# Kernel tuning notes

Hardware: AMD Instinct MI355X
Metric: run time of the kernel (lower is better)

Reference implementation:

```python
import jax, jax.numpy as jnp
import numpy as np

B, NT, S, D, VOCAB = 32, 1024, 4096, 512, 2545


def setup_inputs() -> dict:
    key = jax.random.key(0)
    k1, k2, k3, k4 = jax.random.split(key, 4)
    raw = jax.random.randint(k1, (B, NT), 0, VOCAB, dtype=jnp.int32)
    # per-sample text lengths; trailing positions padded with -1 (-> id 0 after +1)
    text_lens = jax.random.randint(k2, (B,), NT // 2, NT + 1, dtype=jnp.int32)
    pos = jnp.arange(NT, dtype=jnp.int32)[None, :]
    text = jnp.where(pos < text_lens[:, None], raw, -1).astype(jnp.int32)
    # per-sample target (audio) lengths; pin max to S so max_seq_len is static
    seq_len = jax.random.randint(k3, (B,), S // 2, S + 1, dtype=jnp.int32)
    seq_len = seq_len.at[0].set(S)
    # nn.Embedding default init: N(0, 1)
    W_embed = jax.random.normal(k4, (VOCAB + 1, D), dtype=jnp.float32)
    return {"text": text, "seq_len": seq_len, "W_embed": W_embed}


def _upsample_one(emb_i, L, A):
    # emb_i: [S, D]; valid tokens occupy the prefix of length L.
    # Replicates the torch length-regulator: token j repeated base times,
    # plus one extra repeat for the last `remainder` tokens (j >= L - r).
    t = jnp.arange(emb_i.shape[0], dtype=jnp.int32)
    Ls = jnp.maximum(L, 1)
    base = A // Ls
    r = A % Ls
    split = (L - r) * base  # output positions < split map to blocks of size `base`
    j = jnp.where(
        t < split,
        t // jnp.maximum(base, 1),
        (L - r) + (t - split) // (base + 1),
    )
    j = jnp.clip(j, 0, emb_i.shape[0] - 1)
    out = emb_i[j]  # gather from prefix (valid indices are contiguous from 0)
    ok = (t < A)[:, None] & (L > 0) & (A > 0)
    return jnp.where(ok, out, 0.0)


def reference(text, seq_len, W_embed):
    ids = text + 1                                        # [B, NT], pads (-1) -> 0
    ids = jnp.pad(ids, ((0, 0), (0, S - NT)))             # pad to max_seq_len with 0
    pos = jnp.arange(S, dtype=jnp.int32)[None, :]
    valid_pos = pos < seq_len[:, None]                    # [B, S]
    ids = jnp.where(valid_pos, ids, 0)
    text_mask = ids == 0                                  # padding mask
    emb = W_embed[ids]                                    # [B, S, D] embedding lookup
    emb = jnp.where(valid_pos[..., None], emb, 0.0)
    text_lens = jnp.sum(~text_mask, axis=1).astype(jnp.int32)
    return jax.vmap(_upsample_one)(emb, text_lens, seq_len)
```

## Files before the change

### kernel.cpp

```cpp
#include <hip/hip_runtime.h>

#define BB 32
#define NT 1024
#define SS 4096
#define DD 512
#define D4 128

typedef float f32x4 __attribute__((ext_vector_type(4)));

__global__ void prep_kernel(const int* __restrict__ text,
                            const int* __restrict__ seq_len,
                            int4* __restrict__ params) {
    int b = blockIdx.x;
    int tid = threadIdx.x;
    int cnt = 0;
    for (int k = tid; k < NT; k += 256)
        cnt += (text[b * NT + k] >= 0) ? 1 : 0;
    for (int off = 32; off > 0; off >>= 1)
        cnt += __shfl_down(cnt, off);
    __shared__ int s[4];
    if ((tid & 63) == 0) s[tid >> 6] = cnt;
    __syncthreads();
    if (tid == 0) {
        int L = s[0] + s[1] + s[2] + s[3];
        int A = seq_len[b];
        int Ls = (L > 0) ? L : 1;
        int base = A / Ls;
        int rr = A - base * Ls;
        int split = (L - rr) * base;
        params[b] = make_int4(L, base, rr, split);
    }
}

__global__ void __launch_bounds__(256) upsample_kernel(
        const int* __restrict__ text,
        const int* __restrict__ seq_len,
        const f32x4* __restrict__ W4,
        const int4* __restrict__ params,
        f32x4* __restrict__ out4) {
    int idx = blockIdx.x * 256 + threadIdx.x;
    int d4  = idx & (D4 - 1);
    int row = idx >> 7;
    int t   = row & (SS - 1);
    int b   = row >> 12;

    int A = seq_len[b];
    f32x4 v = (f32x4)(0.0f);
    if (t < A) {
        int4 p = params[b];
        int L = p.x, base = p.y, rr = p.z, split = p.w;
        if (L > 0) {
            int j;
            if (t < split) {
                int bb = (base > 0) ? base : 1;
                j = t / bb;
            } else {
                j = (L - rr) + (t - split) / (base + 1);
            }
            if (j > SS - 1) j = SS - 1;
            if (j < 0) j = 0;
            int tok = text[b * NT + j] + 1;
            v = W4[(long)tok * D4 + d4];
        }
    }
    __builtin_nontemporal_store(v, &out4[idx]);
}

extern "C" void kernel_launch(void* const* d_in, const int* in_sizes, int n_in,
                              void* d_out, int out_size, void* d_ws, size_t ws_size,
                              hipStream_t stream) {
    const int* text    = (const int*)d_in[0];
    const int* seq_len = (const int*)d_in[1];
    const f32x4* W4    = (const f32x4*)d_in[2];
    f32x4* out4        = (f32x4*)d_out;
    int4* params       = (int4*)d_ws;

    prep_kernel<<<BB, 256, 0, stream>>>(text, seq_len, params);

    int total = BB * SS * D4;
    upsample_kernel<<<total / 256, 256, 0, stream>>>(text, seq_len, W4, params, out4);
}
```

Before: 52.57 us.

## Fuse length-count prep into upsample kernel via per-wave ballot search

Removes the separate prep kernel and computes each sample's text length inside every wavefront using two ballot passes that locate the first -1 pad. This relies on padding being a contiguous suffix, which the input setup guarantees. Each wave now handles one output row with two vec4 loads and stores per lane, instead of one vec4 per thread. This saves a kernel launch and the dependency between kernels, but adds redundant text reads and ballots per row.

```diff
diff --git a/kernel.cpp b/kernel.cpp
--- a/kernel.cpp
+++ b/kernel.cpp
@@ -1,69 +1,61 @@
 #include <hip/hip_runtime.h>
 
 #define BB 32
-#define NT 1024
+#define NTT 1024
 #define SS 4096
-#define DD 512
 #define D4 128
 
 typedef float f32x4 __attribute__((ext_vector_type(4)));
 
-__global__ void prep_kernel(const int* __restrict__ text,
-                            const int* __restrict__ seq_len,
-                            int4* __restrict__ params) {
-    int b = blockIdx.x;
-    int tid = threadIdx.x;
-    int cnt = 0;
-    for (int k = tid; k < NT; k += 256)
-        cnt += (text[b * NT + k] >= 0) ? 1 : 0;
-    for (int off = 32; off > 0; off >>= 1)
-        cnt += __shfl_down(cnt, off);
-    __shared__ int s[4];
-    if ((tid & 63) == 0) s[tid >> 6] = cnt;
-    __syncthreads();
-    if (tid == 0) {
-        int L = s[0] + s[1] + s[2] + s[3];
-        int A = seq_len[b];
-        int Ls = (L > 0) ? L : 1;
-        int base = A / Ls;
-        int rr = A - base * Ls;
-        int split = (L - rr) * base;
-        params[b] = make_int4(L, base, rr, split);
-    }
-}
-
-__global__ void __launch_bounds__(256) upsample_kernel(
+__global__ void __launch_bounds__(256) fused_upsample_kernel(
         const int* __restrict__ text,
         const int* __restrict__ seq_len,
         const f32x4* __restrict__ W4,
-        const int4* __restrict__ params,
         f32x4* __restrict__ out4) {
-    int idx = blockIdx.x * 256 + threadIdx.x;
-    int d4  = idx & (D4 - 1);
-    int row = idx >> 7;
-    int t   = row & (SS - 1);
-    int b   = row >> 12;
+    int wid  = (blockIdx.x << 2) + (threadIdx.x >> 6);
+    int lane = threadIdx.x & 63;
+    int t = wid & (SS - 1);
+    int b = wid >> 12;
+
+    const int* trow = text + b * NTT;
+
+    int v1 = trow[lane << 4];
+    unsigned long long m1 = __ballot(v1 < 0);
+    int lo;
+    if (m1 == 0ull) {
+        lo = NTT - 16;
+    } else {
+        int p = __builtin_ctzll(m1);
+        lo = (p == 0) ? 0 : ((p - 1) << 4);
+    }
+    int k2 = lo + lane;
+    int v2 = (k2 < NTT) ? trow[k2] : -1;
+    unsigned long long m2 = __ballot(v2 < 0);
+    int L = lo + __builtin_ctzll(m2);
 
     int A = seq_len[b];
-    f32x4 v = (f32x4)(0.0f);
-    if (t < A) {
-        int4 p = params[b];
-        int L = p.x, base = p.y, rr = p.z, split = p.w;
-        if (L > 0) {
-            int j;
-            if (t < split) {
-                int bb = (base > 0) ? base : 1;
-                j = t / bb;
-            } else {
-                j = (L - rr) + (t - split) / (base + 1);
-            }
-            if (j > SS - 1) j = SS - 1;
-            if (j < 0) j = 0;
-            int tok = text[b * NT + j] + 1;
-            v = W4[(long)tok * D4 + d4];
+
+    f32x4 va = (f32x4)(0.0f);
+    f32x4 vb = (f32x4)(0.0f);
+    if (t < A && L > 0) {
+        int base  = (int)((unsigned)A / (unsigned)L);
+        int rr    = A - base * L;
+        int split = (L - rr) * base;
+        int j;
+        if (t < split) {
+            j = (int)((unsigned)t / (unsigned)base);
+        } else {
+            j = (L - rr) + (int)((unsigned)(t - split) / (unsigned)(base + 1));
         }
+        if (j > L - 1) j = L - 1;
+        int tok = trow[j] + 1;
+        const f32x4* wr = W4 + (long)tok * D4;
+        va = wr[lane];
+        vb = wr[lane + 64];
     }
-    __builtin_nontemporal_store(v, &out4[idx]);
+    f32x4* orow = out4 + (long)wid * D4;
+    __builtin_nontemporal_store(va, &orow[lane]);
+    __builtin_nontemporal_store(vb, &orow[lane + 64]);
 }
 
 extern "C" void kernel_launch(void* const* d_in, const int* in_sizes, int n_in,
@@ -73,10 +65,7 @@
     const int* seq_len = (const int*)d_in[1];
     const f32x4* W4    = (const f32x4*)d_in[2];
     f32x4* out4        = (f32x4*)d_out;
-    int4* params       = (int4*)d_ws;
 
-    prep_kernel<<<BB, 256, 0, stream>>>(text, seq_len, params);
-
-    int total = BB * SS * D4;
-    upsample_kernel<<<total / 256, 256, 0, stream>>>(text, seq_len, W4, params, out4);
+    int nblocks = BB * SS / 4;
+    fused_upsample_kernel<<<nblocks, 256, 0, stream>>>(text, seq_len, W4, out4);
 }
```

New measurement: 45.80 us (median of 2 runs). 1.15x faster.
